# Kernel tuning notes

Hardware: AMD Instinct MI355X
Metric: run time of the kernel (lower is better)

## Reference

```python
import jax, jax.numpy as jnp
import numpy as np

T, D, H, E, K = 8192, 1024, 768, 16, 2


def setup_inputs() -> dict:
    key = jax.random.key(0)
    k1, k2, k3, k4, k5, k6 = jax.random.split(key, 6)
    x = jax.random.normal(k1, (T, D), dtype=jnp.float32)
    weights = jax.random.uniform(k2, (T, K), dtype=jnp.float32)
    indices = jax.random.randint(k3, (T, K), 0, E, dtype=jnp.int64)
    counts = jax.random.randint(k4, (E,), 0, 1024, dtype=jnp.int32)
    # GatedMLP params per expert: fc1: D -> 2H (value | gate), fc2: H -> D, no bias
    W1 = jax.random.normal(k5, (E, D, 2 * H), dtype=jnp.float32) * (1.0 / np.sqrt(D))
    W2 = jax.random.normal(k6, (E, H, D), dtype=jnp.float32) * (1.0 / np.sqrt(H))
    return {"x": x, "weights": weights, "indices": indices, "counts": counts, "W1": W1, "W2": W2}


def _gated_mlp(x, w1, w2):
    h = x @ w1                      # [T, 2H]
    v, g = jnp.split(h, 2, axis=-1)  # value, gate halves (torch chunk order)
    return (v * jax.nn.silu(g)) @ w2  # [T, D]


def reference(x, weights, indices, counts, W1, W2):
    # y[t] = sum_k weights[t,k] * GatedMLP_{indices[t,k]}(x[t])
    # Expressed as a masked per-expert combine: w_e[t] = sum_k weights[t,k]*[indices[t,k]==e].
    # Identical math to the torch gather/scatter loop (zero weight -> zero contribution).
    n_experts = W1.shape[0]
    y = jnp.zeros_like(x)
    for e in range(n_experts):
        w_e = jnp.sum(weights * (indices == e), axis=-1)  # [T]
        y = y + _gated_mlp(x, W1[e], W2[e]) * w_e[:, None]
    return y
```

## Files before the change

### kernel.cpp

```cpp
#include <hip/hip_runtime.h>
#include <hip/hip_bf16.h>

#define T_TOK 8192
#define D_DIM 1024
#define H_DIM 768
#define E_EXP 16
#define K_TOP 2
#define TK (T_TOK * K_TOP)
#define NT128 144
#define NT256 80

typedef __bf16 bf16x8 __attribute__((ext_vector_type(8)));
typedef unsigned short u16x8 __attribute__((ext_vector_type(8)));
typedef float f32x4 __attribute__((ext_vector_type(4)));

typedef const __attribute__((address_space(1))) void* gas_t;
typedef __attribute__((address_space(3))) void* las_t;

__device__ __forceinline__ unsigned short f2b(float f) {
    __hip_bfloat16 h = __float2bfloat16(f);
    return __builtin_bit_cast(unsigned short, h);
}
__device__ __forceinline__ float b2f(unsigned short u) {
    unsigned int x = ((unsigned int)u) << 16;
    return __builtin_bit_cast(float, x);
}

__global__ __launch_bounds__(1024) void k_route(
    const int* __restrict__ idx, const float* __restrict__ wts,
    int* __restrict__ offs, int* __restrict__ tiletab, int* __restrict__ tiletab256,
    int* __restrict__ rows, float* __restrict__ wslot, int* __restrict__ slot_of) {
    __shared__ int lcnt[E_EXP];
    __shared__ int lcur[E_EXP];
    const int tid = threadIdx.x;
    if (tid < E_EXP) lcnt[tid] = 0;
    __syncthreads();
    for (int i = tid; i < TK; i += 1024) atomicAdd(&lcnt[idx[i]], 1);
    __syncthreads();
    if (tid == 0) {
        int s = 0, nt = 0, nt2 = 0;
        for (int e = 0; e < E_EXP; ++e) {
            offs[e] = s;
            lcur[e] = s;
            const int n = lcnt[e];
            for (int m0 = 0; m0 < n; m0 += 128) tiletab[nt++] = (e << 16) | (m0 >> 7);
            for (int m0 = 0; m0 < n; m0 += 256) tiletab256[nt2++] = (e << 16) | (m0 >> 8);
            s += n;
        }
        offs[E_EXP] = s;
        for (int i = nt; i < NT128; ++i) tiletab[i] = -1;
        for (int i = nt2; i < NT256; ++i) tiletab256[i] = -1;
    }
    __syncthreads();
    for (int i = tid; i < TK; i += 1024) {
        const int e = idx[i];
        const int p = atomicAdd(&lcur[e], 1);
        rows[p] = i >> 1;
        wslot[p] = wts[i];
        slot_of[i] = p;
    }
}

#define PREP_X T_TOK
#define PREP_W1 (PREP_X + (D_DIM / 64) * ((2 * H_DIM) / 64) * E_EXP)
#define PREP_W2 (PREP_W1 + (H_DIM / 64) * (D_DIM / 64) * E_EXP)

__global__ __launch_bounds__(256) void k_prep(
    const float* __restrict__ x, const float* __restrict__ W1, const float* __restrict__ W2,
    unsigned short* __restrict__ xb, unsigned short* __restrict__ W1T,
    unsigned short* __restrict__ W2T) {
    const int b = blockIdx.x;
    const int tid = threadIdx.x;
    if (b < PREP_X) {
        const int d = tid * 4;
        const float4 v = *reinterpret_cast<const float4*>(&x[(size_t)b * D_DIM + d]);
        ushort4 u;
        u.x = f2b(v.x); u.y = f2b(v.y); u.z = f2b(v.z); u.w = f2b(v.w);
        *reinterpret_cast<ushort4*>(&xb[(size_t)b * D_DIM + d]) = u;
        return;
    }
    __shared__ float t4[64][65];
    const float* src; unsigned short* dst; int K, C, e, kb, cb, pack;
    if (b < PREP_W1) {
        const int q = b - PREP_X;
        K = D_DIM; C = 2 * H_DIM; pack = 1;
        e = q / ((K / 64) * (C / 64));
        const int r = q % ((K / 64) * (C / 64));
        kb = (r % (K / 64)) * 64; cb = (r / (K / 64)) * 64;
        src = W1; dst = W1T;
    } else {
        const int q = b - PREP_W1;
        K = H_DIM; C = D_DIM; pack = 0;
        e = q / ((K / 64) * (C / 64));
        const int r = q % ((K / 64) * (C / 64));
        kb = (r % (K / 64)) * 64; cb = (r / (K / 64)) * 64;
        src = W2; dst = W2T;
    }
    const float* s = src + ((size_t)e * K + kb) * C + cb;
#pragma unroll
    for (int i = 0; i < 4; ++i) {
        const int kk = (tid >> 4) + i * 16, c4 = (tid & 15) * 4;
        const float4 v = *reinterpret_cast<const float4*>(&s[(size_t)kk * C + c4]);
        t4[kk][c4] = v.x; t4[kk][c4 + 1] = v.y; t4[kk][c4 + 2] = v.z; t4[kk][c4 + 3] = v.w;
    }
    __syncthreads();
#pragma unroll
    for (int i = 0; i < 4; ++i) {
        const int cc = (tid >> 4) + i * 16, k4 = (tid & 15) * 4;
        const int j = cb + cc;
        int drow;
        if (pack) drow = (j < H_DIM) ? ((j >> 5) * 64 + (j & 31))
                                     : (((j - H_DIM) >> 5) * 64 + 32 + ((j - H_DIM) & 31));
        else drow = j;
        ushort4 u;
        u.x = f2b(t4[k4][cc]); u.y = f2b(t4[k4 + 1][cc]);
        u.z = f2b(t4[k4 + 2][cc]); u.w = f2b(t4[k4 + 3][cc]);
        *reinterpret_cast<ushort4*>(&dst[((size_t)e * C + drow) * K + kb + k4]) = u;
    }
}


__global__ __launch_bounds__(512, 1) void k_gemm1_fast(
    const unsigned short* __restrict__ xb, const unsigned short* __restrict__ W1T,
    const int* __restrict__ offs, const int* __restrict__ tiletab256,
    const int* __restrict__ rows, unsigned short* __restrict__ act) {
    const int ti = (blockIdx.x & 7) * (NT256 / 8) + (blockIdx.x >> 3);
    const int tt = tiletab256[ti];
    if (tt < 0) return;
    const int e = tt >> 16, m0 = (tt & 0xffff) << 8;
    const int off = offs[e], n_e = offs[e + 1] - off;
    const int by = blockIdx.y;

    __shared__ unsigned short SA[4][256 * 32];
    __shared__ unsigned short SB[4][256 * 32];

    const int tid = threadIdx.x;
    const int wid = tid >> 6, lane = tid & 63;
    const int l15 = lane & 15, kq = lane >> 4;
    const int wm = wid >> 2, wn = wid & 3;
    const int srow_lo = tid >> 2;
    const int esw = (((tid & 3) ^ ((tid >> 3) & 3)) << 3);
    const int rk = ((kq ^ ((l15 >> 1) & 3)) << 3);

    int tok[2];
    long bB[2];
#pragma unroll
    for (int j = 0; j < 2; ++j) {
        int s = m0 + j * 128 + srow_lo;
        s = (s < n_e) ? s : (n_e - 1);
        tok[j] = rows[off + s];
        bB[j] = ((size_t)e * (2 * H_DIM) + by * 256 + j * 128 + srow_lo) * D_DIM + esw;
    }

    f32x4 acc[8][4];
#pragma unroll
    for (int m = 0; m < 8; ++m)
#pragma unroll
        for (int n = 0; n < 4; ++n)
#pragma unroll
            for (int r = 0; r < 4; ++r) acc[m][n][r] = 0.f;

    auto stage = [&](int t) {
        const int sl = t & 3;
        const int k0 = t * 32;
#pragma unroll
        for (int j = 0; j < 2; ++j) {
            const unsigned short* ga = xb + (size_t)tok[j] * D_DIM + k0 + esw;
            __builtin_amdgcn_global_load_lds((gas_t)ga,
                (las_t)((char*)&SA[sl][0] + j * 8192 + tid * 16), 16, 0, 0);
            const unsigned short* gb = W1T + bB[j] + k0;
            __builtin_amdgcn_global_load_lds((gas_t)gb,
                (las_t)((char*)&SB[sl][0] + j * 8192 + tid * 16), 16, 0, 0);
        }
    };

    stage(0); stage(1); stage(2);
    const int NT = D_DIM / 32;
    for (int t = 0; t < NT; ++t) {
        if (t < NT - 2)       asm volatile("s_waitcnt vmcnt(8)" ::: "memory");
        else if (t == NT - 2) asm volatile("s_waitcnt vmcnt(4)" ::: "memory");
        else                  asm volatile("s_waitcnt vmcnt(0)" ::: "memory");
        __builtin_amdgcn_s_barrier();
        asm volatile("" ::: "memory");
        if (t + 3 < NT) stage(t + 3);
        const int sl = t & 3;
        bf16x8 a[8], b[4];
#pragma unroll
        for (int m = 0; m < 8; ++m) {
            const int row = wm * 128 + m * 16 + l15;
            a[m] = __builtin_bit_cast(bf16x8, *reinterpret_cast<const u16x8*>(
                &SA[sl][row * 32 + rk]));
        }
#pragma unroll
        for (int n = 0; n < 4; ++n) {
            const int row = wn * 64 + n * 16 + l15;
            b[n] = __builtin_bit_cast(bf16x8, *reinterpret_cast<const u16x8*>(
                &SB[sl][row * 32 + rk]));
        }
        __builtin_amdgcn_s_setprio(1);
#pragma unroll
        for (int m = 0; m < 8; ++m)
#pragma unroll
            for (int n = 0; n < 4; ++n)
                acc[m][n] = __builtin_amdgcn_mfma_f32_16x16x32_bf16(a[m], b[n], acc[m][n], 0, 0, 0);
        __builtin_amdgcn_s_setprio(0);
    }
#pragma unroll
    for (int m = 0; m < 8; ++m)
#pragma unroll
        for (int r = 0; r < 4; ++r) {
            const int row = wm * 128 + m * 16 + kq * 4 + r;
            if (m0 + row < n_e) {
#pragma unroll
                for (int nv = 0; nv < 2; ++nv) {
                    const int col = by * 128 + wn * 32 + nv * 16 + l15;
                    const float vv = acc[m][nv][r], gg = acc[m][2 + nv][r];
                    const float s = gg / (1.0f + __expf(-gg));
                    act[(size_t)(off + m0 + row) * H_DIM + col] = f2b(vv * s);
                }
            }
        }
}

__global__ __launch_bounds__(512, 1) void k_gemm2_fast(
    const unsigned short* __restrict__ act, const unsigned short* __restrict__ W2T,
    const int* __restrict__ offs, const int* __restrict__ tiletab256,
    const float* __restrict__ wslot, unsigned short* __restrict__ slot_out) {
    const int ti = (blockIdx.x & 7) * (NT256 / 8) + (blockIdx.x >> 3);
    const int tt = tiletab256[ti];
    if (tt < 0) return;
    const int e = tt >> 16, m0 = (tt & 0xffff) << 8;
    const int off = offs[e], n_e = offs[e + 1] - off;
    const int by = blockIdx.y;

    __shared__ unsigned short SA[4][256 * 32];
    __shared__ unsigned short SB[4][256 * 32];

    const int tid = threadIdx.x;
    const int wid = tid >> 6, lane = tid & 63;
    const int l15 = lane & 15, kq = lane >> 4;
    const int wm = wid >> 2, wn = wid & 3;
    const int srow_lo = tid >> 2;
    const int esw = (((tid & 3) ^ ((tid >> 3) & 3)) << 3);
    const int rk = ((kq ^ ((l15 >> 1) & 3)) << 3);

    int slotA[2];
    long bB[2];
#pragma unroll
    for (int j = 0; j < 2; ++j) {
        int s = m0 + j * 128 + srow_lo;
        s = (s < n_e) ? s : (n_e - 1);
        slotA[j] = off + s;
        bB[j] = ((size_t)e * D_DIM + by * 256 + j * 128 + srow_lo) * H_DIM + esw;
    }

    f32x4 acc[8][4];
#pragma unroll
    for (int m = 0; m < 8; ++m)
#pragma unroll
        for (int n = 0; n < 4; ++n)
#pragma unroll
            for (int r = 0; r < 4; ++r) acc[m][n][r] = 0.f;

    auto stage = [&](int t) {
        const int sl = t & 3;
        const int k0 = t * 32;
#pragma unroll
        for (int j = 0; j < 2; ++j) {
            const unsigned short* ga = act + (size_t)slotA[j] * H_DIM + k0 + esw;
            __builtin_amdgcn_global_load_lds((gas_t)ga,
                (las_t)((char*)&SA[sl][0] + j * 8192 + tid * 16), 16, 0, 0);
            const unsigned short* gb = W2T + bB[j] + k0;
            __builtin_amdgcn_global_load_lds((gas_t)gb,
                (las_t)((char*)&SB[sl][0] + j * 8192 + tid * 16), 16, 0, 0);
        }
    };

    stage(0); stage(1); stage(2);
    const int NT = H_DIM / 32;
    for (int t = 0; t < NT; ++t) {
        if (t < NT - 2)       asm volatile("s_waitcnt vmcnt(8)" ::: "memory");
        else if (t == NT - 2) asm volatile("s_waitcnt vmcnt(4)" ::: "memory");
        else                  asm volatile("s_waitcnt vmcnt(0)" ::: "memory");
        __builtin_amdgcn_s_barrier();
        asm volatile("" ::: "memory");
        if (t + 3 < NT) stage(t + 3);
        const int sl = t & 3;
        bf16x8 a[8], b[4];
#pragma unroll
        for (int m = 0; m < 8; ++m) {
            const int row = wm * 128 + m * 16 + l15;
            a[m] = __builtin_bit_cast(bf16x8, *reinterpret_cast<const u16x8*>(
                &SA[sl][row * 32 + rk]));
        }
#pragma unroll
        for (int n = 0; n < 4; ++n) {
            const int row = wn * 64 + n * 16 + l15;
            b[n] = __builtin_bit_cast(bf16x8, *reinterpret_cast<const u16x8*>(
                &SB[sl][row * 32 + rk]));
        }
        __builtin_amdgcn_s_setprio(1);
#pragma unroll
        for (int m = 0; m < 8; ++m)
#pragma unroll
            for (int n = 0; n < 4; ++n)
                acc[m][n] = __builtin_amdgcn_mfma_f32_16x16x32_bf16(a[m], b[n], acc[m][n], 0, 0, 0);
        __builtin_amdgcn_s_setprio(0);
    }
#pragma unroll
    for (int m = 0; m < 8; ++m)
#pragma unroll
        for (int r = 0; r < 4; ++r) {
            const int row = wm * 128 + m * 16 + kq * 4 + r;
            if (m0 + row < n_e) {
                const int slot = off + m0 + row;
                const float w = wslot[slot];
#pragma unroll
                for (int n = 0; n < 4; ++n) {
                    const int col = by * 256 + wn * 64 + n * 16 + l15;
                    slot_out[(size_t)slot * D_DIM + col] = f2b(w * acc[m][n][r]);
                }
            }
        }
}

__global__ __launch_bounds__(256) void k_gather(const float* __restrict__ x,
                                                const int* __restrict__ rows,
                                                unsigned short* __restrict__ xg) {
    const int s = blockIdx.x, t = threadIdx.x;
    const int tok = rows[s];
    const float4 v = *reinterpret_cast<const float4*>(&x[(size_t)tok * D_DIM + t * 4]);
    ushort4 u;
    u.x = f2b(v.x); u.y = f2b(v.y); u.z = f2b(v.z); u.w = f2b(v.w);
    *reinterpret_cast<ushort4*>(&xg[(size_t)s * D_DIM + t * 4]) = u;
}

__global__ __launch_bounds__(256) void k_gemm1_fb(
    const unsigned short* __restrict__ xg, const float* __restrict__ W1,
    const int* __restrict__ offs, const int* __restrict__ tiletab,
    unsigned short* __restrict__ act) {
    const int tt = tiletab[blockIdx.x];
    if (tt < 0) return;
    const int e = tt >> 16, m0 = (tt & 0xffff) << 7;
    const int off = offs[e], n_e = offs[e + 1] - off;
    const int h0 = blockIdx.y * 64;

    __shared__ unsigned short Ab[128 * 64];
    __shared__ unsigned short Bb[128 * 66];

    const int tid = threadIdx.x;
    const int wid = tid >> 6, lane = tid & 63;
    const int l15 = lane & 15, kq = lane >> 4;

    f32x4 acc[2][8];
#pragma unroll
    for (int m = 0; m < 2; ++m)
#pragma unroll
        for (int n = 0; n < 8; ++n)
#pragma unroll
            for (int r = 0; r < 4; ++r) acc[m][n][r] = 0.f;

    for (int k0 = 0; k0 < D_DIM; k0 += 64) {
        __syncthreads();
#pragma unroll
        for (int j = 0; j < 4; ++j) {
            const int o = wid * 4096 + j * 1024 + lane * 16;
            const int row = o >> 7, kb = o & 127;
            int gr = off + m0 + row; gr = (gr < TK) ? gr : (TK - 1);
            const unsigned short* gp = xg + (size_t)gr * D_DIM + k0 + (kb >> 1);
            __builtin_amdgcn_global_load_lds((gas_t)gp,
                (las_t)((char*)Ab + wid * 4096 + j * 1024), 16, 0, 0);
        }
        {
            const float* W1e = W1 + (size_t)e * D_DIM * (2 * H_DIM);
#pragma unroll
            for (int i = 0; i < 8; ++i) {
                const int flat = tid + 256 * i;
                const int cg = flat & 31, kk = flat >> 5;
                const int cc = cg * 4;
                const int gc = (cc < 64) ? (h0 + cc) : (H_DIM + h0 + cc - 64);
                const float4 v = *reinterpret_cast<const float4*>(
                    &W1e[(size_t)(k0 + kk) * (2 * H_DIM) + gc]);
                Bb[(cc + 0) * 66 + kk] = f2b(v.x);
                Bb[(cc + 1) * 66 + kk] = f2b(v.y);
                Bb[(cc + 2) * 66 + kk] = f2b(v.z);
                Bb[(cc + 3) * 66 + kk] = f2b(v.w);
            }
        }
        __syncthreads();
#pragma unroll
        for (int ks = 0; ks < 2; ++ks) {
            bf16x8 a[2], b[8];
#pragma unroll
            for (int m = 0; m < 2; ++m)
                a[m] = __builtin_bit_cast(bf16x8, *reinterpret_cast<const u16x8*>(
                    &Ab[(wid * 32 + m * 16 + l15) * 64 + ks * 32 + kq * 8]));
#pragma unroll
            for (int n = 0; n < 8; ++n)
                b[n] = __builtin_bit_cast(bf16x8, *reinterpret_cast<const u16x8*>(
                    &Bb[(n * 16 + l15) * 66 + ks * 32 + kq * 8]));
#pragma unroll
            for (int m = 0; m < 2; ++m)
#pragma unroll
                for (int n = 0; n < 8; ++n)
                    acc[m][n] = __builtin_amdgcn_mfma_f32_16x16x32_bf16(a[m], b[n], acc[m][n], 0, 0, 0);
        }
    }
#pragma unroll
    for (int m = 0; m < 2; ++m)
#pragma unroll
        for (int n = 0; n < 4; ++n)
#pragma unroll
            for (int r = 0; r < 4; ++r) {
                const int row = wid * 32 + m * 16 + kq * 4 + r;
                if (m0 + row < n_e) {
                    const float vv = acc[m][n][r], gg = acc[m][n + 4][r];
                    const float s = gg / (1.0f + __expf(-gg));
                    act[(size_t)(off + m0 + row) * H_DIM + h0 + n * 16 + l15] = f2b(vv * s);
                }
            }
}

__global__ __launch_bounds__(256) void k_gemm2_fb(
    const unsigned short* __restrict__ act, const float* __restrict__ W2,
    const int* __restrict__ offs, const int* __restrict__ tiletab,
    const float* __restrict__ wslot, unsigned short* __restrict__ slot_out,
    float* __restrict__ y, const int* __restrict__ rows, int atomic_mode) {
    const int tt = tiletab[blockIdx.x];
    if (tt < 0) return;
    const int e = tt >> 16, m0 = (tt & 0xffff) << 7;
    const int off = offs[e], n_e = offs[e + 1] - off;
    const int n0 = blockIdx.y * 64;

    __shared__ unsigned short Ab[128 * 64];
    __shared__ unsigned short Bb[64 * 66];

    const int tid = threadIdx.x;
    const int wid = tid >> 6, lane = tid & 63;
    const int l15 = lane & 15, kq = lane >> 4;

    f32x4 acc[2][4];
#pragma unroll
    for (int m = 0; m < 2; ++m)
#pragma unroll
        for (int n = 0; n < 4; ++n)
#pragma unroll
            for (int r = 0; r < 4; ++r) acc[m][n][r] = 0.f;

    for (int k0 = 0; k0 < H_DIM; k0 += 64) {
        __syncthreads();
#pragma unroll
        for (int j = 0; j < 4; ++j) {
            const int o = wid * 4096 + j * 1024 + lane * 16;
            const int row = o >> 7, kb = o & 127;
            int gr = off + m0 + row; gr = (gr < TK) ? gr : (TK - 1);
            const unsigned short* gp = act + (size_t)gr * H_DIM + k0 + (kb >> 1);
            __builtin_amdgcn_global_load_lds((gas_t)gp,
                (las_t)((char*)Ab + wid * 4096 + j * 1024), 16, 0, 0);
        }
        {
            const float* W2e = W2 + (size_t)e * H_DIM * D_DIM;
#pragma unroll
            for (int i = 0; i < 4; ++i) {
                const int flat = tid + 256 * i;
                const int cg = flat & 15, kk = flat >> 4;
                const int cc = cg * 4;
                const float4 v = *reinterpret_cast<const float4*>(
                    &W2e[(size_t)(k0 + kk) * D_DIM + n0 + cc]);
                Bb[(cc + 0) * 66 + kk] = f2b(v.x);
                Bb[(cc + 1) * 66 + kk] = f2b(v.y);
                Bb[(cc + 2) * 66 + kk] = f2b(v.z);
                Bb[(cc + 3) * 66 + kk] = f2b(v.w);
            }
        }
        __syncthreads();
#pragma unroll
        for (int ks = 0; ks < 2; ++ks) {
            bf16x8 a[2], b[4];
#pragma unroll
            for (int m = 0; m < 2; ++m)
                a[m] = __builtin_bit_cast(bf16x8, *reinterpret_cast<const u16x8*>(
                    &Ab[(wid * 32 + m * 16 + l15) * 64 + ks * 32 + kq * 8]));
#pragma unroll
            for (int n = 0; n < 4; ++n)
                b[n] = __builtin_bit_cast(bf16x8, *reinterpret_cast<const u16x8*>(
                    &Bb[(n * 16 + l15) * 66 + ks * 32 + kq * 8]));
#pragma unroll
            for (int m = 0; m < 2; ++m)
#pragma unroll
                for (int n = 0; n < 4; ++n)
                    acc[m][n] = __builtin_amdgcn_mfma_f32_16x16x32_bf16(a[m], b[n], acc[m][n], 0, 0, 0);
        }
    }
#pragma unroll
    for (int m = 0; m < 2; ++m)
#pragma unroll
        for (int r = 0; r < 4; ++r) {
            const int row = wid * 32 + m * 16 + kq * 4 + r;
            if (m0 + row < n_e) {
                const int slot = off + m0 + row;
                const float w = wslot[slot];
#pragma unroll
                for (int n = 0; n < 4; ++n) {
                    const float o = w * acc[m][n][r];
                    if (atomic_mode)
                        atomicAdd(&y[(size_t)rows[slot] * D_DIM + n0 + n * 16 + l15], o);
                    else
                        slot_out[(size_t)slot * D_DIM + n0 + n * 16 + l15] = f2b(o);
                }
            }
        }
}

__global__ __launch_bounds__(256) void k_combine(
    const unsigned short* __restrict__ slot_out, const int* __restrict__ slot_of,
    float* __restrict__ y) {
    const int t = blockIdx.x;
    const int d = threadIdx.x * 4;
    const int s0 = slot_of[2 * t], s1 = slot_of[2 * t + 1];
    const ushort4 a = *reinterpret_cast<const ushort4*>(&slot_out[(size_t)s0 * D_DIM + d]);
    const ushort4 b = *reinterpret_cast<const ushort4*>(&slot_out[(size_t)s1 * D_DIM + d]);
    float4 r;
    r.x = b2f(a.x) + b2f(b.x);
    r.y = b2f(a.y) + b2f(b.y);
    r.z = b2f(a.z) + b2f(b.z);
    r.w = b2f(a.w) + b2f(b.w);
    *reinterpret_cast<float4*>(&y[(size_t)t * D_DIM + d]) = r;
}

extern "C" void kernel_launch(void* const* d_in, const int* in_sizes, int n_in,
                              void* d_out, int out_size, void* d_ws, size_t ws_size,
                              hipStream_t stream) {
    const float* x = (const float*)d_in[0];
    const float* wts = (const float*)d_in[1];
    const int* idx = (const int*)d_in[2];
    const float* W1 = (const float*)d_in[4];
    const float* W2 = (const float*)d_in[5];
    float* y = (float*)d_out;

    char* ws = (char*)d_ws;
    int* offs = (int*)(ws + 128);
    int* tiletab = (int*)(ws + 320);
    int* tiletab256 = (int*)(ws + 1024);
    int* rows = (int*)(ws + 2048);
    float* wslot = (float*)(ws + 2048 + (size_t)TK * 4);
    int* slot_of = (int*)(ws + 2048 + (size_t)TK * 8);
    const size_t OFF_XG = 2048 + (size_t)TK * 12;
    unsigned short* xg = (unsigned short*)(ws + OFF_XG);
    unsigned short* xb = xg;
    const size_t OFF_ACT = OFF_XG + (size_t)TK * D_DIM * 2;
    unsigned short* act = (unsigned short*)(ws + OFF_ACT);
    const size_t OFF_SO = OFF_ACT + (size_t)TK * H_DIM * 2;
    unsigned short* slot_out = (unsigned short*)(ws + OFF_SO);
    const size_t MID_END = OFF_SO + (size_t)TK * D_DIM * 2;
    const size_t OFF_W1T = MID_END;
    unsigned short* W1T = (unsigned short*)(ws + OFF_W1T);
    const size_t OFF_W2T = OFF_W1T + (size_t)E_EXP * 2 * H_DIM * D_DIM * 2;
    unsigned short* W2T = (unsigned short*)(ws + OFF_W2T);
    const size_t FULL_END = OFF_W2T + (size_t)E_EXP * D_DIM * H_DIM * 2;

    const int full = (ws_size >= FULL_END) ? 1 : 0;
    const int atomic_mode = (!full && ws_size < MID_END) ? 1 : 0;

    k_route<<<1, 1024, 0, stream>>>(idx, wts, offs, tiletab, tiletab256, rows, wslot, slot_of);

    if (full) {
        k_prep<<<PREP_W2, 256, 0, stream>>>(x, W1, W2, xb, W1T, W2T);
        dim3 g1(NT256, H_DIM / 128);
        k_gemm1_fast<<<g1, 512, 0, stream>>>(xb, W1T, offs, tiletab256, rows, act);
        dim3 g2(NT256, D_DIM / 256);
        k_gemm2_fast<<<g2, 512, 0, stream>>>(act, W2T, offs, tiletab256, wslot, slot_out);
        k_combine<<<T_TOK, 256, 0, stream>>>(slot_out, slot_of, y);
    } else {
        k_gather<<<TK, 256, 0, stream>>>(x, rows, xg);
        dim3 g1(NT128, H_DIM / 64);
        k_gemm1_fb<<<g1, 256, 0, stream>>>(xg, W1, offs, tiletab, act);
        if (atomic_mode) hipMemsetAsync(y, 0, (size_t)out_size * 4, stream);
        dim3 g2(NT128, D_DIM / 64);
        k_gemm2_fb<<<g2, 256, 0, stream>>>(act, W2, offs, tiletab, wslot, slot_out, y, rows, atomic_mode);
        if (!atomic_mode)
            k_combine<<<T_TOK, 256, 0, stream>>>(slot_out, slot_of, y);
    }
}
```

Measured before the change: 254.3 us.

## Restructure MoE GEMM main loops into phased double-buffered pipeline with interleaved staging

Both grouped GEMM kernels switch from a 4-slot, 32-wide K ring buffer to a 2-slot double buffer of 64-wide K tiles, each split into two 32-wide halves. Each half runs as two MFMA phases of 4x4 tiles. The A and B global-to-LDS loads for the next tile are issued between these phases, with explicit barriers, sched_barrier and priority changes around each phase. The aim is to interleave memory issue with MFMA work and reduce register pressure by holding only 4 A fragments at a time. In exchange it adds more barriers per K step and leaves less prefetch depth than the old three-stage lookahead.

Result: faster. 244.9 us (-3.7%).

```diff
diff --git a/kernel.cpp b/kernel.cpp
--- a/kernel.cpp
+++ b/kernel.cpp
@@ -120,6 +120,42 @@
 }
 
 
+#define PH_OPEN()                                          \
+    asm volatile("" ::: "memory");                         \
+    __builtin_amdgcn_s_barrier();                          \
+    asm volatile("s_waitcnt lgkmcnt(0)" ::: "memory");     \
+    __builtin_amdgcn_sched_barrier(0);                     \
+    __builtin_amdgcn_s_setprio(1);
+
+#define PH_CLOSE()                                         \
+    __builtin_amdgcn_s_setprio(0);                         \
+    asm volatile("" ::: "memory");                         \
+    __builtin_amdgcn_s_barrier();
+
+#define MM4(BASE)                                                          \
+    _Pragma("unroll")                                                      \
+    for (int mf = 0; mf < 4; ++mf)                                         \
+        _Pragma("unroll")                                                  \
+        for (int nf = 0; nf < 4; ++nf)                                     \
+            acc[(BASE) + mf][nf] = __builtin_amdgcn_mfma_f32_16x16x32_bf16( \
+                a[mf], b[nf], acc[(BASE) + mf][nf], 0, 0, 0);
+
+#define LDA4(SL, KS, MG)                                                   \
+    _Pragma("unroll")                                                      \
+    for (int mf = 0; mf < 4; ++mf) {                                       \
+        const int row_ = wm * 128 + (MG) * 64 + mf * 16 + l15;             \
+        a[mf] = __builtin_bit_cast(bf16x8, *reinterpret_cast<const u16x8*>( \
+            &SA[(((SL) * 2 + (KS)) * 256 + row_) * 32 + rk]));             \
+    }
+
+#define LDB4(SL, KS)                                                       \
+    _Pragma("unroll")                                                      \
+    for (int nf = 0; nf < 4; ++nf) {                                       \
+        const int row_ = wn * 64 + nf * 16 + l15;                          \
+        b[nf] = __builtin_bit_cast(bf16x8, *reinterpret_cast<const u16x8*>( \
+            &SB[(((SL) * 2 + (KS)) * 256 + row_) * 32 + rk]));             \
+    }
+
 __global__ __launch_bounds__(512, 1) void k_gemm1_fast(
     const unsigned short* __restrict__ xb, const unsigned short* __restrict__ W1T,
     const int* __restrict__ offs, const int* __restrict__ tiletab256,
@@ -131,25 +167,25 @@
     const int off = offs[e], n_e = offs[e + 1] - off;
     const int by = blockIdx.y;
 
-    __shared__ unsigned short SA[4][256 * 32];
-    __shared__ unsigned short SB[4][256 * 32];
+    __shared__ unsigned short SA[2 * 2 * 256 * 32];
+    __shared__ unsigned short SB[2 * 2 * 256 * 32];
 
     const int tid = threadIdx.x;
     const int wid = tid >> 6, lane = tid & 63;
     const int l15 = lane & 15, kq = lane >> 4;
     const int wm = wid >> 2, wn = wid & 3;
-    const int srow_lo = tid >> 2;
+    const int row_lo = tid >> 2;
     const int esw = (((tid & 3) ^ ((tid >> 3) & 3)) << 3);
     const int rk = ((kq ^ ((l15 >> 1) & 3)) << 3);
 
     int tok[2];
-    long bB[2];
+    size_t bB[2];
 #pragma unroll
     for (int j = 0; j < 2; ++j) {
-        int s = m0 + j * 128 + srow_lo;
+        int s = m0 + j * 128 + row_lo;
         s = (s < n_e) ? s : (n_e - 1);
         tok[j] = rows[off + s];
-        bB[j] = ((size_t)e * (2 * H_DIM) + by * 256 + j * 128 + srow_lo) * D_DIM + esw;
+        bB[j] = ((size_t)e * (2 * H_DIM) + by * 256 + j * 128 + row_lo) * D_DIM + esw;
     }
 
     f32x4 acc[8][4];
@@ -160,50 +196,63 @@
 #pragma unroll
             for (int r = 0; r < 4; ++r) acc[m][n][r] = 0.f;
 
-    auto stage = [&](int t) {
-        const int sl = t & 3;
-        const int k0 = t * 32;
+    auto STAGE_A = [&](int sl, int ks, int t) {
 #pragma unroll
         for (int j = 0; j < 2; ++j) {
-            const unsigned short* ga = xb + (size_t)tok[j] * D_DIM + k0 + esw;
+            const unsigned short* ga = xb + (size_t)tok[j] * D_DIM + t * 64 + ks * 32 + esw;
             __builtin_amdgcn_global_load_lds((gas_t)ga,
-                (las_t)((char*)&SA[sl][0] + j * 8192 + tid * 16), 16, 0, 0);
-            const unsigned short* gb = W1T + bB[j] + k0;
+                (las_t)((char*)SA + ((sl * 2 + ks) * 256 + j * 128) * 64 + tid * 16), 16, 0, 0);
+        }
+    };
+    auto STAGE_B = [&](int sl, int ks, int t) {
+#pragma unroll
+        for (int j = 0; j < 2; ++j) {
+            const unsigned short* gb = W1T + bB[j] + t * 64 + ks * 32;
             __builtin_amdgcn_global_load_lds((gas_t)gb,
-                (las_t)((char*)&SB[sl][0] + j * 8192 + tid * 16), 16, 0, 0);
+                (las_t)((char*)SB + ((sl * 2 + ks) * 256 + j * 128) * 64 + tid * 16), 16, 0, 0);
         }
     };
 
-    stage(0); stage(1); stage(2);
-    const int NT = D_DIM / 32;
-    for (int t = 0; t < NT; ++t) {
-        if (t < NT - 2)       asm volatile("s_waitcnt vmcnt(8)" ::: "memory");
-        else if (t == NT - 2) asm volatile("s_waitcnt vmcnt(4)" ::: "memory");
-        else                  asm volatile("s_waitcnt vmcnt(0)" ::: "memory");
+    STAGE_A(0, 0, 0); STAGE_B(0, 0, 0); STAGE_A(0, 1, 0); STAGE_B(0, 1, 0);
+    asm volatile("s_waitcnt vmcnt(4)" ::: "memory");
+    asm volatile("" ::: "memory");
+    __builtin_amdgcn_s_barrier();
+
+    const int NTILE = D_DIM / 64;
+    bf16x8 a[4], b[4];
+    for (int t = 0; t < NTILE; ++t) {
+        const int sl = t & 1, sn = sl ^ 1;
+        const int tn = t + 1;
+        const bool st = (tn < NTILE);
+        LDB4(sl, 0);
+        LDA4(sl, 0, 0);
+        if (st) STAGE_A(sn, 0, tn);
+        PH_OPEN();
+        MM4(0);
+        PH_CLOSE();
+        LDA4(sl, 0, 1);
+        if (st) STAGE_B(sn, 0, tn);
+        PH_OPEN();
+        MM4(4);
+        __builtin_amdgcn_s_setprio(0);
+        if (st) { asm volatile("s_waitcnt vmcnt(4)" ::: "memory"); }
+        else    { asm volatile("s_waitcnt vmcnt(0)" ::: "memory"); }
+        asm volatile("" ::: "memory");
         __builtin_amdgcn_s_barrier();
+        LDB4(sl, 1);
+        LDA4(sl, 1, 0);
+        if (st) STAGE_A(sn, 1, tn);
+        PH_OPEN();
+        MM4(0);
+        PH_CLOSE();
+        LDA4(sl, 1, 1);
+        if (st) STAGE_B(sn, 1, tn);
+        PH_OPEN();
+        MM4(4);
+        __builtin_amdgcn_s_setprio(0);
+        if (st) { asm volatile("s_waitcnt vmcnt(4)" ::: "memory"); }
         asm volatile("" ::: "memory");
-        if (t + 3 < NT) stage(t + 3);
-        const int sl = t & 3;
-        bf16x8 a[8], b[4];
-#pragma unroll
-        for (int m = 0; m < 8; ++m) {
-            const int row = wm * 128 + m * 16 + l15;
-            a[m] = __builtin_bit_cast(bf16x8, *reinterpret_cast<const u16x8*>(
-                &SA[sl][row * 32 + rk]));
-        }
-#pragma unroll
-        for (int n = 0; n < 4; ++n) {
-            const int row = wn * 64 + n * 16 + l15;
-            b[n] = __builtin_bit_cast(bf16x8, *reinterpret_cast<const u16x8*>(
-                &SB[sl][row * 32 + rk]));
-        }
-        __builtin_amdgcn_s_setprio(1);
-#pragma unroll
-        for (int m = 0; m < 8; ++m)
-#pragma unroll
-            for (int n = 0; n < 4; ++n)
-                acc[m][n] = __builtin_amdgcn_mfma_f32_16x16x32_bf16(a[m], b[n], acc[m][n], 0, 0, 0);
-        __builtin_amdgcn_s_setprio(0);
+        __builtin_amdgcn_s_barrier();
     }
 #pragma unroll
     for (int m = 0; m < 8; ++m)
@@ -233,25 +282,25 @@
     const int off = offs[e], n_e = offs[e + 1] - off;
     const int by = blockIdx.y;
 
-    __shared__ unsigned short SA[4][256 * 32];
-    __shared__ unsigned short SB[4][256 * 32];
+    __shared__ unsigned short SA[2 * 2 * 256 * 32];
+    __shared__ unsigned short SB[2 * 2 * 256 * 32];
 
     const int tid = threadIdx.x;
     const int wid = tid >> 6, lane = tid & 63;
     const int l15 = lane & 15, kq = lane >> 4;
     const int wm = wid >> 2, wn = wid & 3;
-    const int srow_lo = tid >> 2;
+    const int row_lo = tid >> 2;
     const int esw = (((tid & 3) ^ ((tid >> 3) & 3)) << 3);
     const int rk = ((kq ^ ((l15 >> 1) & 3)) << 3);
 
     int slotA[2];
-    long bB[2];
+    size_t bB[2];
 #pragma unroll
     for (int j = 0; j < 2; ++j) {
-        int s = m0 + j * 128 + srow_lo;
+        int s = m0 + j * 128 + row_lo;
         s = (s < n_e) ? s : (n_e - 1);
         slotA[j] = off + s;
-        bB[j] = ((size_t)e * D_DIM + by * 256 + j * 128 + srow_lo) * H_DIM + esw;
+        bB[j] = ((size_t)e * D_DIM + by * 256 + j * 128 + row_lo) * H_DIM + esw;
     }
 
     f32x4 acc[8][4];
@@ -262,50 +311,63 @@
 #pragma unroll
             for (int r = 0; r < 4; ++r) acc[m][n][r] = 0.f;
 
-    auto stage = [&](int t) {
-        const int sl = t & 3;
-        const int k0 = t * 32;
+    auto STAGE_A = [&](int sl, int ks, int t) {
 #pragma unroll
         for (int j = 0; j < 2; ++j) {
-            const unsigned short* ga = act + (size_t)slotA[j] * H_DIM + k0 + esw;
+            const unsigned short* ga = act + (size_t)slotA[j] * H_DIM + t * 64 + ks * 32 + esw;
             __builtin_amdgcn_global_load_lds((gas_t)ga,
-                (las_t)((char*)&SA[sl][0] + j * 8192 + tid * 16), 16, 0, 0);
-            const unsigned short* gb = W2T + bB[j] + k0;
+                (las_t)((char*)SA + ((sl * 2 + ks) * 256 + j * 128) * 64 + tid * 16), 16, 0, 0);
+        }
+    };
+    auto STAGE_B = [&](int sl, int ks, int t) {
+#pragma unroll
+        for (int j = 0; j < 2; ++j) {
+            const unsigned short* gb = W2T + bB[j] + t * 64 + ks * 32;
             __builtin_amdgcn_global_load_lds((gas_t)gb,
-                (las_t)((char*)&SB[sl][0] + j * 8192 + tid * 16), 16, 0, 0);
+                (las_t)((char*)SB + ((sl * 2 + ks) * 256 + j * 128) * 64 + tid * 16), 16, 0, 0);
         }
     };
 
-    stage(0); stage(1); stage(2);
-    const int NT = H_DIM / 32;
-    for (int t = 0; t < NT; ++t) {
-        if (t < NT - 2)       asm volatile("s_waitcnt vmcnt(8)" ::: "memory");
-        else if (t == NT - 2) asm volatile("s_waitcnt vmcnt(4)" ::: "memory");
-        else                  asm volatile("s_waitcnt vmcnt(0)" ::: "memory");
+    STAGE_A(0, 0, 0); STAGE_B(0, 0, 0); STAGE_A(0, 1, 0); STAGE_B(0, 1, 0);
+    asm volatile("s_waitcnt vmcnt(4)" ::: "memory");
+    asm volatile("" ::: "memory");
+    __builtin_amdgcn_s_barrier();
+
+    const int NTILE = H_DIM / 64;
+    bf16x8 a[4], b[4];
+    for (int t = 0; t < NTILE; ++t) {
+        const int sl = t & 1, sn = sl ^ 1;
+        const int tn = t + 1;
+        const bool st = (tn < NTILE);
+        LDB4(sl, 0);
+        LDA4(sl, 0, 0);
+        if (st) STAGE_A(sn, 0, tn);
+        PH_OPEN();
+        MM4(0);
+        PH_CLOSE();
+        LDA4(sl, 0, 1);
+        if (st) STAGE_B(sn, 0, tn);
+        PH_OPEN();
+        MM4(4);
+        __builtin_amdgcn_s_setprio(0);
+        if (st) { asm volatile("s_waitcnt vmcnt(4)" ::: "memory"); }
+        else    { asm volatile("s_waitcnt vmcnt(0)" ::: "memory"); }
+        asm volatile("" ::: "memory");
         __builtin_amdgcn_s_barrier();
+        LDB4(sl, 1);
+        LDA4(sl, 1, 0);
+        if (st) STAGE_A(sn, 1, tn);
+        PH_OPEN();
+        MM4(0);
+        PH_CLOSE();
+        LDA4(sl, 1, 1);
+        if (st) STAGE_B(sn, 1, tn);
+        PH_OPEN();
+        MM4(4);
+        __builtin_amdgcn_s_setprio(0);
+        if (st) { asm volatile("s_waitcnt vmcnt(4)" ::: "memory"); }
         asm volatile("" ::: "memory");
-        if (t + 3 < NT) stage(t + 3);
-        const int sl = t & 3;
-        bf16x8 a[8], b[4];
-#pragma unroll
-        for (int m = 0; m < 8; ++m) {
-            const int row = wm * 128 + m * 16 + l15;
-            a[m] = __builtin_bit_cast(bf16x8, *reinterpret_cast<const u16x8*>(
-                &SA[sl][row * 32 + rk]));
-        }
-#pragma unroll
-        for (int n = 0; n < 4; ++n) {
-            const int row = wn * 64 + n * 16 + l15;
-            b[n] = __builtin_bit_cast(bf16x8, *reinterpret_cast<const u16x8*>(
-                &SB[sl][row * 32 + rk]));
-        }
-        __builtin_amdgcn_s_setprio(1);
-#pragma unroll
-        for (int m = 0; m < 8; ++m)
-#pragma unroll
-            for (int n = 0; n < 4; ++n)
-                acc[m][n] = __builtin_amdgcn_mfma_f32_16x16x32_bf16(a[m], b[n], acc[m][n], 0, 0, 0);
-        __builtin_amdgcn_s_setprio(0);
+        __builtin_amdgcn_s_barrier();
     }
 #pragma unroll
     for (int m = 0; m < 8; ++m)
```

## Shrink grouped GEMM tiles to 128 rows with double-buffered LDS and two blocks per CU

Applied to the files above, without the earlier changes.

Both expert GEMM kernels move from 256-row M tiles with a 4-stage global_load_lds ring and hand-tuned vmcnt waits to 128-row tiles with simple double buffering and __syncthreads. The 256-row tile table is dropped and the 128-row table is reused, so the grid has more, smaller blocks. Launch bounds now ask for two blocks per CU. The aim is less padding waste on partly filled expert tiles and better occupancy and load balance. In exchange, the weight tiles are reused across fewer rows, and the shallower pipeline with a full barrier every k-step may expose memory latency.

After: 212.2 us. 16.5% less time.

```diff
diff --git a/kernel.cpp b/kernel.cpp
--- a/kernel.cpp
+++ b/kernel.cpp
@@ -28,7 +28,7 @@
 
 __global__ __launch_bounds__(1024) void k_route(
     const int* __restrict__ idx, const float* __restrict__ wts,
-    int* __restrict__ offs, int* __restrict__ tiletab, int* __restrict__ tiletab256,
+    int* __restrict__ offs, int* __restrict__ tiletab,
     int* __restrict__ rows, float* __restrict__ wslot, int* __restrict__ slot_of) {
     __shared__ int lcnt[E_EXP];
     __shared__ int lcur[E_EXP];
@@ -38,18 +38,16 @@
     for (int i = tid; i < TK; i += 1024) atomicAdd(&lcnt[idx[i]], 1);
     __syncthreads();
     if (tid == 0) {
-        int s = 0, nt = 0, nt2 = 0;
+        int s = 0, nt = 0;
         for (int e = 0; e < E_EXP; ++e) {
             offs[e] = s;
             lcur[e] = s;
             const int n = lcnt[e];
             for (int m0 = 0; m0 < n; m0 += 128) tiletab[nt++] = (e << 16) | (m0 >> 7);
-            for (int m0 = 0; m0 < n; m0 += 256) tiletab256[nt2++] = (e << 16) | (m0 >> 8);
             s += n;
         }
         offs[E_EXP] = s;
         for (int i = nt; i < NT128; ++i) tiletab[i] = -1;
-        for (int i = nt2; i < NT256; ++i) tiletab256[i] = -1;
     }
     __syncthreads();
     for (int i = tid; i < TK; i += 1024) {
@@ -120,96 +118,87 @@
 }
 
 
-__global__ __launch_bounds__(512, 1) void k_gemm1_fast(
+__global__ __launch_bounds__(512, 2) void k_gemm1_fast(
     const unsigned short* __restrict__ xb, const unsigned short* __restrict__ W1T,
-    const int* __restrict__ offs, const int* __restrict__ tiletab256,
+    const int* __restrict__ offs, const int* __restrict__ tiletab,
     const int* __restrict__ rows, unsigned short* __restrict__ act) {
-    const int ti = (blockIdx.x & 7) * (NT256 / 8) + (blockIdx.x >> 3);
-    const int tt = tiletab256[ti];
+    const int ti = (blockIdx.x & 7) * (NT128 / 8) + (blockIdx.x >> 3);
+    const int tt = tiletab[ti];
     if (tt < 0) return;
-    const int e = tt >> 16, m0 = (tt & 0xffff) << 8;
+    const int e = tt >> 16, m0 = (tt & 0xffff) << 7;
     const int off = offs[e], n_e = offs[e + 1] - off;
     const int by = blockIdx.y;
 
-    __shared__ unsigned short SA[4][256 * 32];
-    __shared__ unsigned short SB[4][256 * 32];
+    __shared__ unsigned short SA[2][128 * 32];
+    __shared__ unsigned short SB[2][256 * 32];
 
     const int tid = threadIdx.x;
     const int wid = tid >> 6, lane = tid & 63;
     const int l15 = lane & 15, kq = lane >> 4;
     const int wm = wid >> 2, wn = wid & 3;
-    const int srow_lo = tid >> 2;
+    const int srow = tid >> 2;
     const int esw = (((tid & 3) ^ ((tid >> 3) & 3)) << 3);
     const int rk = ((kq ^ ((l15 >> 1) & 3)) << 3);
 
-    int tok[2];
-    long bB[2];
-#pragma unroll
-    for (int j = 0; j < 2; ++j) {
-        int s = m0 + j * 128 + srow_lo;
-        s = (s < n_e) ? s : (n_e - 1);
-        tok[j] = rows[off + s];
-        bB[j] = ((size_t)e * (2 * H_DIM) + by * 256 + j * 128 + srow_lo) * D_DIM + esw;
-    }
-
-    f32x4 acc[8][4];
-#pragma unroll
-    for (int m = 0; m < 8; ++m)
+    int tok;
+    { int s = m0 + srow; s = (s < n_e) ? s : (n_e - 1); tok = rows[off + s]; }
+    size_t bB[2];
+#pragma unroll
+    for (int j = 0; j < 2; ++j)
+        bB[j] = ((size_t)e * (2 * H_DIM) + by * 256 + j * 128 + srow) * D_DIM + esw;
+
+    f32x4 acc[4][4];
+#pragma unroll
+    for (int m = 0; m < 4; ++m)
 #pragma unroll
         for (int n = 0; n < 4; ++n)
 #pragma unroll
             for (int r = 0; r < 4; ++r) acc[m][n][r] = 0.f;
 
-    auto stage = [&](int t) {
-        const int sl = t & 3;
-        const int k0 = t * 32;
+    auto stage = [&](int buf, int k0) {
+        const unsigned short* ga = xb + (size_t)tok * D_DIM + k0 + esw;
+        __builtin_amdgcn_global_load_lds((gas_t)ga,
+            (las_t)((char*)&SA[buf][0] + tid * 16), 16, 0, 0);
 #pragma unroll
         for (int j = 0; j < 2; ++j) {
-            const unsigned short* ga = xb + (size_t)tok[j] * D_DIM + k0 + esw;
-            __builtin_amdgcn_global_load_lds((gas_t)ga,
-                (las_t)((char*)&SA[sl][0] + j * 8192 + tid * 16), 16, 0, 0);
             const unsigned short* gb = W1T + bB[j] + k0;
             __builtin_amdgcn_global_load_lds((gas_t)gb,
-                (las_t)((char*)&SB[sl][0] + j * 8192 + tid * 16), 16, 0, 0);
+                (las_t)((char*)&SB[buf][0] + j * 8192 + tid * 16), 16, 0, 0);
         }
     };
 
-    stage(0); stage(1); stage(2);
+    stage(0, 0);
+    __syncthreads();
+    int c = 0;
     const int NT = D_DIM / 32;
     for (int t = 0; t < NT; ++t) {
-        if (t < NT - 2)       asm volatile("s_waitcnt vmcnt(8)" ::: "memory");
-        else if (t == NT - 2) asm volatile("s_waitcnt vmcnt(4)" ::: "memory");
-        else                  asm volatile("s_waitcnt vmcnt(0)" ::: "memory");
-        __builtin_amdgcn_s_barrier();
-        asm volatile("" ::: "memory");
-        if (t + 3 < NT) stage(t + 3);
-        const int sl = t & 3;
-        bf16x8 a[8], b[4];
-#pragma unroll
-        for (int m = 0; m < 8; ++m) {
-            const int row = wm * 128 + m * 16 + l15;
+        if (t + 1 < NT) stage(c ^ 1, (t + 1) * 32);
+        bf16x8 a[4], b[4];
+#pragma unroll
+        for (int m = 0; m < 4; ++m) {
+            const int row = wm * 64 + m * 16 + l15;
             a[m] = __builtin_bit_cast(bf16x8, *reinterpret_cast<const u16x8*>(
-                &SA[sl][row * 32 + rk]));
+                &SA[c][row * 32 + rk]));
         }
 #pragma unroll
         for (int n = 0; n < 4; ++n) {
             const int row = wn * 64 + n * 16 + l15;
             b[n] = __builtin_bit_cast(bf16x8, *reinterpret_cast<const u16x8*>(
-                &SB[sl][row * 32 + rk]));
-        }
-        __builtin_amdgcn_s_setprio(1);
-#pragma unroll
-        for (int m = 0; m < 8; ++m)
+                &SB[c][row * 32 + rk]));
+        }
+#pragma unroll
+        for (int m = 0; m < 4; ++m)
 #pragma unroll
             for (int n = 0; n < 4; ++n)
                 acc[m][n] = __builtin_amdgcn_mfma_f32_16x16x32_bf16(a[m], b[n], acc[m][n], 0, 0, 0);
-        __builtin_amdgcn_s_setprio(0);
-    }
-#pragma unroll
-    for (int m = 0; m < 8; ++m)
+        __syncthreads();
+        c ^= 1;
+    }
+#pragma unroll
+    for (int m = 0; m < 4; ++m)
 #pragma unroll
         for (int r = 0; r < 4; ++r) {
-            const int row = wm * 128 + m * 16 + kq * 4 + r;
+            const int row = wm * 64 + m * 16 + kq * 4 + r;
             if (m0 + row < n_e) {
 #pragma unroll
                 for (int nv = 0; nv < 2; ++nv) {
@@ -222,96 +211,87 @@
         }
 }
 
-__global__ __launch_bounds__(512, 1) void k_gemm2_fast(
+__global__ __launch_bounds__(512, 2) void k_gemm2_fast(
     const unsigned short* __restrict__ act, const unsigned short* __restrict__ W2T,
-    const int* __restrict__ offs, const int* __restrict__ tiletab256,
+    const int* __restrict__ offs, const int* __restrict__ tiletab,
     const float* __restrict__ wslot, unsigned short* __restrict__ slot_out) {
-    const int ti = (blockIdx.x & 7) * (NT256 / 8) + (blockIdx.x >> 3);
-    const int tt = tiletab256[ti];
+    const int ti = (blockIdx.x & 7) * (NT128 / 8) + (blockIdx.x >> 3);
+    const int tt = tiletab[ti];
     if (tt < 0) return;
-    const int e = tt >> 16, m0 = (tt & 0xffff) << 8;
+    const int e = tt >> 16, m0 = (tt & 0xffff) << 7;
     const int off = offs[e], n_e = offs[e + 1] - off;
     const int by = blockIdx.y;
 
-    __shared__ unsigned short SA[4][256 * 32];
-    __shared__ unsigned short SB[4][256 * 32];
+    __shared__ unsigned short SA[2][128 * 32];
+    __shared__ unsigned short SB[2][256 * 32];
 
     const int tid = threadIdx.x;
     const int wid = tid >> 6, lane = tid & 63;
     const int l15 = lane & 15, kq = lane >> 4;
     const int wm = wid >> 2, wn = wid & 3;
-    const int srow_lo = tid >> 2;
+    const int srow = tid >> 2;
     const int esw = (((tid & 3) ^ ((tid >> 3) & 3)) << 3);
     const int rk = ((kq ^ ((l15 >> 1) & 3)) << 3);
 
-    int slotA[2];
-    long bB[2];
-#pragma unroll
-    for (int j = 0; j < 2; ++j) {
-        int s = m0 + j * 128 + srow_lo;
-        s = (s < n_e) ? s : (n_e - 1);
-        slotA[j] = off + s;
-        bB[j] = ((size_t)e * D_DIM + by * 256 + j * 128 + srow_lo) * H_DIM + esw;
-    }
-
-    f32x4 acc[8][4];
-#pragma unroll
-    for (int m = 0; m < 8; ++m)
+    int slotA;
+    { int s = m0 + srow; s = (s < n_e) ? s : (n_e - 1); slotA = off + s; }
+    size_t bB[2];
+#pragma unroll
+    for (int j = 0; j < 2; ++j)
+        bB[j] = ((size_t)e * D_DIM + by * 256 + j * 128 + srow) * H_DIM + esw;
+
+    f32x4 acc[4][4];
+#pragma unroll
+    for (int m = 0; m < 4; ++m)
 #pragma unroll
         for (int n = 0; n < 4; ++n)
 #pragma unroll
             for (int r = 0; r < 4; ++r) acc[m][n][r] = 0.f;
 
-    auto stage = [&](int t) {
-        const int sl = t & 3;
-        const int k0 = t * 32;
+    auto stage = [&](int buf, int k0) {
+        const unsigned short* ga = act + (size_t)slotA * H_DIM + k0 + esw;
+        __builtin_amdgcn_global_load_lds((gas_t)ga,
+            (las_t)((char*)&SA[buf][0] + tid * 16), 16, 0, 0);
 #pragma unroll
         for (int j = 0; j < 2; ++j) {
-            const unsigned short* ga = act + (size_t)slotA[j] * H_DIM + k0 + esw;
-            __builtin_amdgcn_global_load_lds((gas_t)ga,
-                (las_t)((char*)&SA[sl][0] + j * 8192 + tid * 16), 16, 0, 0);
             const unsigned short* gb = W2T + bB[j] + k0;
             __builtin_amdgcn_global_load_lds((gas_t)gb,
-                (las_t)((char*)&SB[sl][0] + j * 8192 + tid * 16), 16, 0, 0);
+                (las_t)((char*)&SB[buf][0] + j * 8192 + tid * 16), 16, 0, 0);
         }
     };
 
-    stage(0); stage(1); stage(2);
+    stage(0, 0);
+    __syncthreads();
+    int c = 0;
     const int NT = H_DIM / 32;
     for (int t = 0; t < NT; ++t) {
-        if (t < NT - 2)       asm volatile("s_waitcnt vmcnt(8)" ::: "memory");
-        else if (t == NT - 2) asm volatile("s_waitcnt vmcnt(4)" ::: "memory");
-        else                  asm volatile("s_waitcnt vmcnt(0)" ::: "memory");
-        __builtin_amdgcn_s_barrier();
-        asm volatile("" ::: "memory");
-        if (t + 3 < NT) stage(t + 3);
-        const int sl = t & 3;
-        bf16x8 a[8], b[4];
-#pragma unroll
-        for (int m = 0; m < 8; ++m) {
-            const int row = wm * 128 + m * 16 + l15;
+        if (t + 1 < NT) stage(c ^ 1, (t + 1) * 32);
+        bf16x8 a[4], b[4];
+#pragma unroll
+        for (int m = 0; m < 4; ++m) {
+            const int row = wm * 64 + m * 16 + l15;
             a[m] = __builtin_bit_cast(bf16x8, *reinterpret_cast<const u16x8*>(
-                &SA[sl][row * 32 + rk]));
+                &SA[c][row * 32 + rk]));
         }
 #pragma unroll
         for (int n = 0; n < 4; ++n) {
             const int row = wn * 64 + n * 16 + l15;
             b[n] = __builtin_bit_cast(bf16x8, *reinterpret_cast<const u16x8*>(
-                &SB[sl][row * 32 + rk]));
-        }
-        __builtin_amdgcn_s_setprio(1);
-#pragma unroll
-        for (int m = 0; m < 8; ++m)
+                &SB[c][row * 32 + rk]));
+        }
+#pragma unroll
+        for (int m = 0; m < 4; ++m)
 #pragma unroll
             for (int n = 0; n < 4; ++n)
                 acc[m][n] = __builtin_amdgcn_mfma_f32_16x16x32_bf16(a[m], b[n], acc[m][n], 0, 0, 0);
-        __builtin_amdgcn_s_setprio(0);
-    }
-#pragma unroll
-    for (int m = 0; m < 8; ++m)
+        __syncthreads();
+        c ^= 1;
+    }
+#pragma unroll
+    for (int m = 0; m < 4; ++m)
 #pragma unroll
         for (int r = 0; r < 4; ++r) {
-            const int row = wm * 128 + m * 16 + kq * 4 + r;
+            const int row = wm * 64 + m * 16 + kq * 4 + r;
             if (m0 + row < n_e) {
                 const int slot = off + m0 + row;
                 const float w = wslot[slot];
@@ -541,7 +521,6 @@
     char* ws = (char*)d_ws;
     int* offs = (int*)(ws + 128);
     int* tiletab = (int*)(ws + 320);
-    int* tiletab256 = (int*)(ws + 1024);
     int* rows = (int*)(ws + 2048);
     float* wslot = (float*)(ws + 2048 + (size_t)TK * 4);
     int* slot_of = (int*)(ws + 2048 + (size_t)TK * 8);
@@ -562,14 +541,14 @@
     const int full = (ws_size >= FULL_END) ? 1 : 0;
     const int atomic_mode = (!full && ws_size < MID_END) ? 1 : 0;
 
-    k_route<<<1, 1024, 0, stream>>>(idx, wts, offs, tiletab, tiletab256, rows, wslot, slot_of);
+    k_route<<<1, 1024, 0, stream>>>(idx, wts, offs, tiletab, rows, wslot, slot_of);
 
     if (full) {
         k_prep<<<PREP_W2, 256, 0, stream>>>(x, W1, W2, xb, W1T, W2T);
-        dim3 g1(NT256, H_DIM / 128);
-        k_gemm1_fast<<<g1, 512, 0, stream>>>(xb, W1T, offs, tiletab256, rows, act);
-        dim3 g2(NT256, D_DIM / 256);
-        k_gemm2_fast<<<g2, 512, 0, stream>>>(act, W2T, offs, tiletab256, wslot, slot_out);
+        dim3 g1(NT128, H_DIM / 128);
+        k_gemm1_fast<<<g1, 512, 0, stream>>>(xb, W1T, offs, tiletab, rows, act);
+        dim3 g2(NT128, D_DIM / 256);
+        k_gemm2_fast<<<g2, 512, 0, stream>>>(act, W2T, offs, tiletab, wslot, slot_out);
         k_combine<<<T_TOK, 256, 0, stream>>>(slot_out, slot_of, y);
     } else {
         k_gather<<<TK, 256, 0, stream>>>(x, rows, xg);
```
